# Optimization experiments

Measured on AMD Instinct MI355X. Metric: run time of the kernel, lower is better.

The kernel has to match this reference:

```python
import jax, jax.numpy as jnp
import numpy as np

NUM_CLASS = 1000
FEAT_DIM = 512
BATCH = 131072


def _safe_cdist(a, b):
    # Euclidean distance matrix, numerically safe sqrt (0 on the diagonal,
    # finite gradient), matching torch.cdist(p=2).
    a2 = jnp.sum(a * a, axis=-1, keepdims=True)        # [Na, 1]
    b2 = jnp.sum(b * b, axis=-1)                       # [Nb]
    d2 = jnp.maximum(a2 + b2 - 2.0 * (a @ b.T), 0.0)   # [Na, Nb]
    pos = d2 > 0
    return jnp.where(pos, jnp.sqrt(jnp.where(pos, d2, 1.0)), 0.0)


def setup_inputs() -> dict:
    key = jax.random.key(0)
    kf, kl, kc = jax.random.split(key, 3)
    features = jax.random.normal(kf, (BATCH, FEAT_DIM), dtype=jnp.float32)
    labels = jax.random.randint(kl, (BATCH,), 0, NUM_CLASS)
    center = jax.random.normal(kc, (NUM_CLASS, FEAT_DIM), dtype=jnp.float32)
    return {"features": features, "center": center, "labels": labels}


def reference(features, center, labels):
    # Threshold computed from the initial centers in __init__ (detached).
    init_dist = _safe_cdist(center, center)                     # [C, C]
    thres_inter = jax.lax.stop_gradient(jnp.mean(init_dist)) * 3.0

    # Per-class accumulation: the Python loops in the torch code are exactly
    # a segment-sum (scatter-add) of features into centers + a bincount.
    counts = jax.ops.segment_sum(
        jnp.ones((labels.shape[0],), dtype=features.dtype), labels,
        num_segments=NUM_CLASS)                                  # [C]
    sums = jax.ops.segment_sum(features, labels, num_segments=NUM_CLASS)  # [C, D]
    new_center = (center + sums) / jnp.maximum(counts, 1.0)[:, None]

    dist = _safe_cdist(new_center, new_center)                   # [C, C]
    hinge = jnp.where(dist < thres_inter, thres_inter - dist, 0.0)
    inter_loss = jnp.mean(hinge)
    # torch forward returns (inter_loss, self.center.data) -- center was
    # mutated in place, so it is the updated per-class mean center.
    return (inter_loss, new_center)
```

## Files before the change

kernel.cpp:

```cpp
#include <hip/hip_runtime.h>
#include <hip/hip_bf16.h>
#include <math.h>

#define BATCH   131072
#define NCLASS  1000
#define FDIM    512
#define NTILE   136
#define CAP     320

typedef __attribute__((ext_vector_type(4))) float f32x4;
typedef __attribute__((ext_vector_type(8))) short short8;

#define OFF_CURSOR   0
#define OFF_ACCS     4096
#define OFF_DONE     4104
#define OFF_PERM     8192
#define OFF_WSM      1290240
static_assert(OFF_PERM + NCLASS * CAP * 4 <= OFF_WSM, "perm/wsM overlap");
static_assert(OFF_ACCS >= OFF_CURSOR + 1024 * 4, "cursor/accs overlap");

__device__ __forceinline__ ushort f2bf(float x) {
    union { float f; unsigned u; } v; v.f = x;
    unsigned r = v.u + 0x7fff + ((v.u >> 16) & 1);
    return (ushort)(r >> 16);
}

template <int MODE>
__device__ void dist_mfma(const float* __restrict__ M, float th, int by, int bx,
                          float* __restrict__ accs) {
    __shared__ ushort Abf[64][72];
    __shared__ ushort Bbf[64][72];
    __shared__ float  rnA[64];
    __shared__ float  rnB[64];
    __shared__ float  red[256];

    const int tid  = threadIdx.x;
    const int lane = tid & 63;
    const int w    = tid >> 6;
    const int wr   = w >> 1, wc = w & 1;
    const int row4 = tid >> 2;
    const int cq   = tid & 3;
    const int gi_s = by * 64 + row4;
    const int gj_s = bx * 64 + row4;

    f32x4 acc[2][2];
#pragma unroll
    for (int m = 0; m < 2; ++m)
#pragma unroll
        for (int n = 0; n < 2; ++n) acc[m][n] = (f32x4){0.f, 0.f, 0.f, 0.f};

    float nA = 0.f, nB = 0.f;
    for (int k0 = 0; k0 < 8; ++k0) {
        __syncthreads();
#pragma unroll
        for (int c = 0; c < 4; ++c) {
            const int col  = cq * 16 + c * 4;
            const int gcol = k0 * 64 + col;
            f32x4 av = (f32x4){0.f, 0.f, 0.f, 0.f};
            f32x4 bv = (f32x4){0.f, 0.f, 0.f, 0.f};
            if (gi_s < NCLASS) av = *(const f32x4*)&M[(size_t)gi_s * FDIM + gcol];
            if (gj_s < NCLASS) bv = *(const f32x4*)&M[(size_t)gj_s * FDIM + gcol];
            nA += av.x * av.x + av.y * av.y + av.z * av.z + av.w * av.w;
            nB += bv.x * bv.x + bv.y * bv.y + bv.z * bv.z + bv.w * bv.w;
            ushort4 ap, bp;
            ap.x = f2bf(av.x); ap.y = f2bf(av.y); ap.z = f2bf(av.z); ap.w = f2bf(av.w);
            bp.x = f2bf(bv.x); bp.y = f2bf(bv.y); bp.z = f2bf(bv.z); bp.w = f2bf(bv.w);
            *(ushort4*)&Abf[row4][col] = ap;
            *(ushort4*)&Bbf[row4][col] = bp;
        }
        __syncthreads();
#pragma unroll
        for (int kk = 0; kk < 2; ++kk) {
            short8 a[2], b[2];
#pragma unroll
            for (int m = 0; m < 2; ++m)
                a[m] = *(const short8*)&Abf[wr * 32 + m * 16 + (lane & 15)]
                                          [kk * 32 + (lane >> 4) * 8];
#pragma unroll
            for (int n = 0; n < 2; ++n)
                b[n] = *(const short8*)&Bbf[wc * 32 + n * 16 + (lane & 15)]
                                          [kk * 32 + (lane >> 4) * 8];
#pragma unroll
            for (int m = 0; m < 2; ++m)
#pragma unroll
                for (int n = 0; n < 2; ++n)
                    acc[m][n] = __builtin_amdgcn_mfma_f32_16x16x32_bf16(
                        a[m], b[n], acc[m][n], 0, 0, 0);
        }
    }

    nA += __shfl_xor(nA, 1, 64); nA += __shfl_xor(nA, 2, 64);
    nB += __shfl_xor(nB, 1, 64); nB += __shfl_xor(nB, 2, 64);
    if (cq == 0) { rnA[row4] = nA; rnB[row4] = nB; }
    __syncthreads();

    float local = 0.f;
#pragma unroll
    for (int m = 0; m < 2; ++m)
#pragma unroll
        for (int n = 0; n < 2; ++n)
#pragma unroll
            for (int i = 0; i < 4; ++i) {
                const int r_l = wr * 32 + m * 16 + (lane >> 4) * 4 + i;
                const int c_l = wc * 32 + n * 16 + (lane & 15);
                const int gi = by * 64 + r_l;
                const int gj = bx * 64 + c_l;
                if (gi < NCLASS && gj < NCLASS && gj > gi) {
                    float d2 = rnA[r_l] + rnB[c_l] - 2.0f * acc[m][n][i];
                    d2 = fmaxf(d2, 0.0f);
                    float dst = (d2 > 0.0f) ? sqrtf(d2) : 0.0f;
                    if (MODE == 1) {
                        if (dst < th) local += th - dst;
                    } else {
                        local += dst;
                    }
                }
            }

    red[tid] = local;
    __syncthreads();
    for (int s = 128; s > 0; s >>= 1) {
        if (tid < s) red[tid] += red[tid + s];
        __syncthreads();
    }
    if (tid == 0) atomicAdd(&accs[MODE], red[0]);
}

__global__ __launch_bounds__(256)
void k2_scatter_dist0(const int* __restrict__ labels,
                      int* __restrict__ cursor0,
                      int* __restrict__ perm,
                      const float* __restrict__ center,
                      float* __restrict__ accs) {
    const int b = blockIdx.x, t = threadIdx.x;
    if (b >= BATCH / 1024) {
        int idx = b - BATCH / 1024;
        int by = 0;
        while (idx >= 16 - by) { idx -= 16 - by; ++by; }
        dist_mfma<0>(center, 0.0f, by, by + idx, accs);
        return;
    }
    const int gid = b * 256 + t;
    int4 l = ((const int4*)labels)[gid];
    const int r = gid * 4;
    perm[l.x * CAP + atomicAdd(&cursor0[l.x], 1)] = r + 0;
    perm[l.y * CAP + atomicAdd(&cursor0[l.y], 1)] = r + 1;
    perm[l.z * CAP + atomicAdd(&cursor0[l.z], 1)] = r + 2;
    perm[l.w * CAP + atomicAdd(&cursor0[l.w], 1)] = r + 3;
}

__global__ __launch_bounds__(512)
void k3_gather_finalize(const float* __restrict__ features,
                        const int* __restrict__ cursor0,
                        const int* __restrict__ perm,
                        const float* __restrict__ center,
                        float* __restrict__ out_center,
                        float* __restrict__ wsM) {
    const int c = blockIdx.x, t = threadIdx.x;
    const int par = t >> 7;
    const int pos = t & 127;
    const int n   = cursor0[c];
    const int* pp = perm + c * CAP;
    __shared__ float part[4][128][4];

    f32x4 acc = (f32x4){0.f, 0.f, 0.f, 0.f};
    int idx[8];
    int r = par;
    if (r + 28 < n) {
#pragma unroll
        for (int u = 0; u < 8; ++u) idx[u] = pp[r + 4 * u];
    }
    while (r + 28 < n) {
        const int nr = r + 32;
        int nidx[8];
        if (nr + 28 < n) {
#pragma unroll
            for (int u = 0; u < 8; ++u) nidx[u] = pp[nr + 4 * u];
        } else {
#pragma unroll
            for (int u = 0; u < 8; ++u) nidx[u] = 0;
        }
        f32x4 v0 = *(const f32x4*)&features[(size_t)idx[0] * FDIM + pos * 4];
        f32x4 v1 = *(const f32x4*)&features[(size_t)idx[1] * FDIM + pos * 4];
        f32x4 v2 = *(const f32x4*)&features[(size_t)idx[2] * FDIM + pos * 4];
        f32x4 v3 = *(const f32x4*)&features[(size_t)idx[3] * FDIM + pos * 4];
        f32x4 v4 = *(const f32x4*)&features[(size_t)idx[4] * FDIM + pos * 4];
        f32x4 v5 = *(const f32x4*)&features[(size_t)idx[5] * FDIM + pos * 4];
        f32x4 v6 = *(const f32x4*)&features[(size_t)idx[6] * FDIM + pos * 4];
        f32x4 v7 = *(const f32x4*)&features[(size_t)idx[7] * FDIM + pos * 4];
        acc += ((v0 + v1) + (v2 + v3)) + ((v4 + v5) + (v6 + v7));
#pragma unroll
        for (int u = 0; u < 8; ++u) idx[u] = nidx[u];
        r = nr;
    }
    for (; r < n; r += 4)
        acc += *(const f32x4*)&features[(size_t)pp[r] * FDIM + pos * 4];

    *(f32x4*)&part[par][pos][0] = acc;
    __syncthreads();
    if (t < 128) {
        f32x4 s = *(const f32x4*)&part[0][t][0];
        s += *(const f32x4*)&part[1][t][0];
        s += *(const f32x4*)&part[2][t][0];
        s += *(const f32x4*)&part[3][t][0];
        const f32x4 cc = *(const f32x4*)&center[(size_t)c * FDIM + t * 4];
        const float invn = 1.0f / fmaxf((float)n, 1.0f);
        const f32x4 nc = (cc + s) * invn;
        float* o = out_center + (size_t)c * FDIM + t * 4;
        o[0] = nc.x; o[1] = nc.y; o[2] = nc.z; o[3] = nc.w;
        *(f32x4*)&wsM[(size_t)c * FDIM + t * 4] = nc;
    }
}

__global__ __launch_bounds__(256)
void k5_dist1(const float* __restrict__ wsM, float* __restrict__ accs,
              int* __restrict__ done, float* __restrict__ out0) {
    int idx = blockIdx.x;
    int by = 0;
    while (idx >= 16 - by) { idx -= 16 - by; ++by; }
    const float th = 6.0f * accs[0] * 1e-6f;
    dist_mfma<1>(wsM, th, by, by + idx, accs);
    if (threadIdx.x == 0) {
        __threadfence();
        if (atomicAdd(done, 1) == NTILE - 1) {
            __threadfence();
            const float l1 = atomicAdd(&accs[1], 0.0f);
            const double thd = 6.0 * (double)accs[0] * 1e-6;
            out0[0] = (float)((2.0 * (double)l1 + (double)NCLASS * thd) * 1e-6);
        }
    }
}

extern "C" void kernel_launch(void* const* d_in, const int* in_sizes, int n_in,
                              void* d_out, int out_size, void* d_ws, size_t ws_size,
                              hipStream_t stream) {
    const float* features = (const float*)d_in[0];
    const float* center   = (const float*)d_in[1];
    const int*   labels   = (const int*)d_in[2];
    float* out = (float*)d_out;
    char*  ws  = (char*)d_ws;

    int*   cursor0 = (int*)(ws + OFF_CURSOR);
    float* accs    = (float*)(ws + OFF_ACCS);
    int*   done    = (int*)(ws + OFF_DONE);
    int*   perm    = (int*)(ws + OFF_PERM);
    float* wsM     = (float*)(ws + OFF_WSM);

    hipMemsetAsync(ws, 0, 4112, stream);
    k2_scatter_dist0<<<BATCH / 1024 + NTILE, 256, 0, stream>>>(labels, cursor0,
                                                               perm, center, accs);
    k3_gather_finalize<<<NCLASS, 512, 0, stream>>>(features, cursor0, perm,
                                                   center, out + 1, wsM);
    k5_dist1<<<NTILE, 256, 0, stream>>>(wsM, accs, done, out);
}
```

Measured before the change: 118.3 us.

## Split per-class gather into quarter work items via persistent atomic work queue

The per-class gather kernel now runs as 1024 persistent blocks that pull work items from a global atomic counter. Each item covers a quarter of one class's rows, which spreads uneven class sizes across blocks. Partial sums go into a zeroed global accumulator with float atomics, and a new small kernel applies the center add and the divide. The cost is a larger memset (about 2 MB), 2M float atomics, an extra launch, and a sum order that is no longer deterministic.

```diff
diff --git a/kernel.cpp b/kernel.cpp
--- a/kernel.cpp
+++ b/kernel.cpp
@@ -7,17 +7,22 @@
 #define FDIM    512
 #define NTILE   136
 #define CAP     320
+#define NITEMS  (4 * NCLASS)
+#define K3BLK   1024
 
 typedef __attribute__((ext_vector_type(4))) float f32x4;
 typedef __attribute__((ext_vector_type(8))) short short8;
 
-#define OFF_CURSOR   0
-#define OFF_ACCS     4096
-#define OFF_DONE     4104
-#define OFF_PERM     8192
-#define OFF_WSM      1290240
+#define OFF_QHEAD    0
+#define OFF_CURSOR   64
+#define OFF_ACCS     4160
+#define OFF_DONE     4168
+#define OFF_ACCBUF   8192
+#define OFF_PERM     2056192
+#define OFF_WSM      3336192
+static_assert(OFF_CURSOR + 1024 * 4 <= OFF_ACCS, "cursor/accs overlap");
+static_assert(OFF_ACCBUF + NCLASS * FDIM * 4 <= OFF_PERM, "accbuf/perm overlap");
 static_assert(OFF_PERM + NCLASS * CAP * 4 <= OFF_WSM, "perm/wsM overlap");
-static_assert(OFF_ACCS >= OFF_CURSOR + 1024 * 4, "cursor/accs overlap");
 
 __device__ __forceinline__ ushort f2bf(float x) {
     union { float f; unsigned u; } v; v.f = x;
@@ -150,66 +155,95 @@
 }
 
 __global__ __launch_bounds__(512)
-void k3_gather_finalize(const float* __restrict__ features,
+void k3_gather_balanced(const float* __restrict__ features,
                         const int* __restrict__ cursor0,
                         const int* __restrict__ perm,
-                        const float* __restrict__ center,
-                        float* __restrict__ out_center,
-                        float* __restrict__ wsM) {
-    const int c = blockIdx.x, t = threadIdx.x;
+                        int* __restrict__ qhead,
+                        float* __restrict__ accbuf) {
+    const int t   = threadIdx.x;
     const int par = t >> 7;
     const int pos = t & 127;
-    const int n   = cursor0[c];
-    const int* pp = perm + c * CAP;
+    __shared__ int   sItem;
     __shared__ float part[4][128][4];
 
-    f32x4 acc = (f32x4){0.f, 0.f, 0.f, 0.f};
-    int idx[8];
-    int r = par;
-    if (r + 28 < n) {
-#pragma unroll
-        for (int u = 0; u < 8; ++u) idx[u] = pp[r + 4 * u];
-    }
-    while (r + 28 < n) {
-        const int nr = r + 32;
-        int nidx[8];
-        if (nr + 28 < n) {
-#pragma unroll
-            for (int u = 0; u < 8; ++u) nidx[u] = pp[nr + 4 * u];
-        } else {
-#pragma unroll
-            for (int u = 0; u < 8; ++u) nidx[u] = 0;
-        }
-        f32x4 v0 = *(const f32x4*)&features[(size_t)idx[0] * FDIM + pos * 4];
-        f32x4 v1 = *(const f32x4*)&features[(size_t)idx[1] * FDIM + pos * 4];
-        f32x4 v2 = *(const f32x4*)&features[(size_t)idx[2] * FDIM + pos * 4];
-        f32x4 v3 = *(const f32x4*)&features[(size_t)idx[3] * FDIM + pos * 4];
-        f32x4 v4 = *(const f32x4*)&features[(size_t)idx[4] * FDIM + pos * 4];
-        f32x4 v5 = *(const f32x4*)&features[(size_t)idx[5] * FDIM + pos * 4];
-        f32x4 v6 = *(const f32x4*)&features[(size_t)idx[6] * FDIM + pos * 4];
-        f32x4 v7 = *(const f32x4*)&features[(size_t)idx[7] * FDIM + pos * 4];
-        acc += ((v0 + v1) + (v2 + v3)) + ((v4 + v5) + (v6 + v7));
-#pragma unroll
-        for (int u = 0; u < 8; ++u) idx[u] = nidx[u];
-        r = nr;
-    }
-    for (; r < n; r += 4)
-        acc += *(const f32x4*)&features[(size_t)pp[r] * FDIM + pos * 4];
-
-    *(f32x4*)&part[par][pos][0] = acc;
-    __syncthreads();
-    if (t < 128) {
-        f32x4 s = *(const f32x4*)&part[0][t][0];
-        s += *(const f32x4*)&part[1][t][0];
-        s += *(const f32x4*)&part[2][t][0];
-        s += *(const f32x4*)&part[3][t][0];
-        const f32x4 cc = *(const f32x4*)&center[(size_t)c * FDIM + t * 4];
-        const float invn = 1.0f / fmaxf((float)n, 1.0f);
-        const f32x4 nc = (cc + s) * invn;
-        float* o = out_center + (size_t)c * FDIM + t * 4;
-        o[0] = nc.x; o[1] = nc.y; o[2] = nc.z; o[3] = nc.w;
-        *(f32x4*)&wsM[(size_t)c * FDIM + t * 4] = nc;
-    }
+    for (;;) {
+        if (t == 0) sItem = atomicAdd(qhead, 1);
+        __syncthreads();
+        const int item = sItem;
+        if (item >= NITEMS) break;
+        const int c  = item % NCLASS;
+        const int qt = item / NCLASS;
+        const int n   = cursor0[c];
+        const int per = (n + 3) >> 2;
+        const int s0  = qt * per;
+        const int e0  = min(n, s0 + per);
+        const int cnt = e0 - s0;
+        const int* pp = perm + c * CAP + s0;
+
+        f32x4 acc = (f32x4){0.f, 0.f, 0.f, 0.f};
+        int idx[8];
+        int r = par;
+        if (r + 28 < cnt) {
+#pragma unroll
+            for (int u = 0; u < 8; ++u) idx[u] = pp[r + 4 * u];
+        }
+        while (r + 28 < cnt) {
+            const int nr = r + 32;
+            int nidx[8];
+            if (nr + 28 < cnt) {
+#pragma unroll
+                for (int u = 0; u < 8; ++u) nidx[u] = pp[nr + 4 * u];
+            } else {
+#pragma unroll
+                for (int u = 0; u < 8; ++u) nidx[u] = 0;
+            }
+            f32x4 v0 = *(const f32x4*)&features[(size_t)idx[0] * FDIM + pos * 4];
+            f32x4 v1 = *(const f32x4*)&features[(size_t)idx[1] * FDIM + pos * 4];
+            f32x4 v2 = *(const f32x4*)&features[(size_t)idx[2] * FDIM + pos * 4];
+            f32x4 v3 = *(const f32x4*)&features[(size_t)idx[3] * FDIM + pos * 4];
+            f32x4 v4 = *(const f32x4*)&features[(size_t)idx[4] * FDIM + pos * 4];
+            f32x4 v5 = *(const f32x4*)&features[(size_t)idx[5] * FDIM + pos * 4];
+            f32x4 v6 = *(const f32x4*)&features[(size_t)idx[6] * FDIM + pos * 4];
+            f32x4 v7 = *(const f32x4*)&features[(size_t)idx[7] * FDIM + pos * 4];
+            acc += ((v0 + v1) + (v2 + v3)) + ((v4 + v5) + (v6 + v7));
+#pragma unroll
+            for (int u = 0; u < 8; ++u) idx[u] = nidx[u];
+            r = nr;
+        }
+        for (; r < cnt; r += 4)
+            acc += *(const f32x4*)&features[(size_t)pp[r] * FDIM + pos * 4];
+
+        *(f32x4*)&part[par][pos][0] = acc;
+        __syncthreads();
+        if (t < 128) {
+            f32x4 s = *(const f32x4*)&part[0][t][0];
+            s += *(const f32x4*)&part[1][t][0];
+            s += *(const f32x4*)&part[2][t][0];
+            s += *(const f32x4*)&part[3][t][0];
+            float* dst = accbuf + (size_t)c * FDIM + t * 4;
+            atomicAdd(dst + 0, s.x);
+            atomicAdd(dst + 1, s.y);
+            atomicAdd(dst + 2, s.z);
+            atomicAdd(dst + 3, s.w);
+        }
+        __syncthreads();
+    }
+}
+
+__global__ __launch_bounds__(128)
+void k4_finalize(const float* __restrict__ center,
+                 const float* __restrict__ accbuf,
+                 const int* __restrict__ cursor0,
+                 float* __restrict__ out_center,
+                 float* __restrict__ wsM) {
+    const int c = blockIdx.x, t = threadIdx.x;
+    const f32x4 s  = *(const f32x4*)&accbuf[(size_t)c * FDIM + t * 4];
+    const f32x4 cc = *(const f32x4*)&center[(size_t)c * FDIM + t * 4];
+    const float invn = 1.0f / fmaxf((float)cursor0[c], 1.0f);
+    const f32x4 nc = (cc + s) * invn;
+    float* o = out_center + (size_t)c * FDIM + t * 4;
+    o[0] = nc.x; o[1] = nc.y; o[2] = nc.z; o[3] = nc.w;
+    *(f32x4*)&wsM[(size_t)c * FDIM + t * 4] = nc;
 }
 
 __global__ __launch_bounds__(256)
@@ -240,16 +274,19 @@
     float* out = (float*)d_out;
     char*  ws  = (char*)d_ws;
 
+    int*   qhead   = (int*)(ws + OFF_QHEAD);
     int*   cursor0 = (int*)(ws + OFF_CURSOR);
     float* accs    = (float*)(ws + OFF_ACCS);
     int*   done    = (int*)(ws + OFF_DONE);
+    float* accbuf  = (float*)(ws + OFF_ACCBUF);
     int*   perm    = (int*)(ws + OFF_PERM);
     float* wsM     = (float*)(ws + OFF_WSM);
 
-    hipMemsetAsync(ws, 0, 4112, stream);
+    hipMemsetAsync(ws, 0, OFF_ACCBUF + NCLASS * FDIM * 4, stream);
     k2_scatter_dist0<<<BATCH / 1024 + NTILE, 256, 0, stream>>>(labels, cursor0,
                                                                perm, center, accs);
-    k3_gather_finalize<<<NCLASS, 512, 0, stream>>>(features, cursor0, perm,
-                                                   center, out + 1, wsM);
+    k3_gather_balanced<<<K3BLK, 512, 0, stream>>>(features, cursor0, perm,
+                                                  qhead, accbuf);
+    k4_finalize<<<NCLASS, 128, 0, stream>>>(center, accbuf, cursor0, out + 1, wsM);
     k5_dist1<<<NTILE, 256, 0, stream>>>(wsM, accs, done, out);
 }
```

New measurement: 155.3 us. +31.3%, slower.

## Split per-class gather across two blocks and add separate finalize kernel

Applied to the files above, without the earlier changes.

The gather kernel now launches two blocks per class, each summing half of that class's feature rows into a partial buffer in workspace. A new small kernel then adds the two partials to the center, divides by the count, and writes the output and the workspace copy. The aim is more blocks in flight to hide memory latency during the gather, at the cost of an extra kernel launch and an extra round trip of about 4 MB of partial sums through global memory.

```diff
diff --git a/kernel.cpp b/kernel.cpp
--- a/kernel.cpp
+++ b/kernel.cpp
@@ -15,8 +15,10 @@
 #define OFF_ACCS     4096
 #define OFF_DONE     4104
 #define OFF_PERM     8192
-#define OFF_WSM      1290240
-static_assert(OFF_PERM + NCLASS * CAP * 4 <= OFF_WSM, "perm/wsM overlap");
+#define OFF_PBUF     1290240
+#define OFF_WSM      5386240
+static_assert(OFF_PERM + NCLASS * CAP * 4 <= OFF_PBUF, "perm/pbuf overlap");
+static_assert(OFF_PBUF + 2 * NCLASS * FDIM * 4 <= OFF_WSM, "pbuf/wsM overlap");
 static_assert(OFF_ACCS >= OFF_CURSOR + 1024 * 4, "cursor/accs overlap");
 
 __device__ __forceinline__ ushort f2bf(float x) {
@@ -150,30 +152,32 @@
 }
 
 __global__ __launch_bounds__(512)
-void k3_gather_finalize(const float* __restrict__ features,
-                        const int* __restrict__ cursor0,
-                        const int* __restrict__ perm,
-                        const float* __restrict__ center,
-                        float* __restrict__ out_center,
-                        float* __restrict__ wsM) {
-    const int c = blockIdx.x, t = threadIdx.x;
+void k3_gather(const float* __restrict__ features,
+               const int* __restrict__ cursor0,
+               const int* __restrict__ perm,
+               float* __restrict__ pbuf) {
+    const int c = blockIdx.x, h = blockIdx.y, t = threadIdx.x;
     const int par = t >> 7;
     const int pos = t & 127;
     const int n   = cursor0[c];
-    const int* pp = perm + c * CAP;
+    const int per = (n + 1) >> 1;
+    const int s0  = h * per;
+    const int e0  = min(n, s0 + per);
+    const int cnt = e0 - s0;
+    const int* pp = perm + c * CAP + s0;
     __shared__ float part[4][128][4];
 
     f32x4 acc = (f32x4){0.f, 0.f, 0.f, 0.f};
     int idx[8];
     int r = par;
-    if (r + 28 < n) {
+    if (r + 28 < cnt) {
 #pragma unroll
         for (int u = 0; u < 8; ++u) idx[u] = pp[r + 4 * u];
     }
-    while (r + 28 < n) {
+    while (r + 28 < cnt) {
         const int nr = r + 32;
         int nidx[8];
-        if (nr + 28 < n) {
+        if (nr + 28 < cnt) {
 #pragma unroll
             for (int u = 0; u < 8; ++u) nidx[u] = pp[nr + 4 * u];
         } else {
@@ -193,7 +197,7 @@
         for (int u = 0; u < 8; ++u) idx[u] = nidx[u];
         r = nr;
     }
-    for (; r < n; r += 4)
+    for (; r < cnt; r += 4)
         acc += *(const f32x4*)&features[(size_t)pp[r] * FDIM + pos * 4];
 
     *(f32x4*)&part[par][pos][0] = acc;
@@ -203,13 +207,25 @@
         s += *(const f32x4*)&part[1][t][0];
         s += *(const f32x4*)&part[2][t][0];
         s += *(const f32x4*)&part[3][t][0];
-        const f32x4 cc = *(const f32x4*)&center[(size_t)c * FDIM + t * 4];
-        const float invn = 1.0f / fmaxf((float)n, 1.0f);
-        const f32x4 nc = (cc + s) * invn;
-        float* o = out_center + (size_t)c * FDIM + t * 4;
-        o[0] = nc.x; o[1] = nc.y; o[2] = nc.z; o[3] = nc.w;
-        *(f32x4*)&wsM[(size_t)c * FDIM + t * 4] = nc;
-    }
+        *(f32x4*)&pbuf[((size_t)h * NCLASS + c) * FDIM + t * 4] = s;
+    }
+}
+
+__global__ __launch_bounds__(128)
+void k4_finalize(const float* __restrict__ center,
+                 const float* __restrict__ pbuf,
+                 const int* __restrict__ cursor0,
+                 float* __restrict__ out_center,
+                 float* __restrict__ wsM) {
+    const int c = blockIdx.x, t = threadIdx.x;
+    f32x4 s = *(const f32x4*)&pbuf[((size_t)0 * NCLASS + c) * FDIM + t * 4];
+    s += *(const f32x4*)&pbuf[((size_t)1 * NCLASS + c) * FDIM + t * 4];
+    const f32x4 cc = *(const f32x4*)&center[(size_t)c * FDIM + t * 4];
+    const float invn = 1.0f / fmaxf((float)cursor0[c], 1.0f);
+    const f32x4 nc = (cc + s) * invn;
+    float* o = out_center + (size_t)c * FDIM + t * 4;
+    o[0] = nc.x; o[1] = nc.y; o[2] = nc.z; o[3] = nc.w;
+    *(f32x4*)&wsM[(size_t)c * FDIM + t * 4] = nc;
 }
 
 __global__ __launch_bounds__(256)
@@ -244,12 +260,13 @@
     float* accs    = (float*)(ws + OFF_ACCS);
     int*   done    = (int*)(ws + OFF_DONE);
     int*   perm    = (int*)(ws + OFF_PERM);
+    float* pbuf    = (float*)(ws + OFF_PBUF);
     float* wsM     = (float*)(ws + OFF_WSM);
 
     hipMemsetAsync(ws, 0, 4112, stream);
     k2_scatter_dist0<<<BATCH / 1024 + NTILE, 256, 0, stream>>>(labels, cursor0,
                                                                perm, center, accs);
-    k3_gather_finalize<<<NCLASS, 512, 0, stream>>>(features, cursor0, perm,
-                                                   center, out + 1, wsM);
+    k3_gather<<<dim3(NCLASS, 2), 512, 0, stream>>>(features, cursor0, perm, pbuf);
+    k4_finalize<<<NCLASS, 128, 0, stream>>>(center, pbuf, cursor0, out + 1, wsM);
     k5_dist1<<<NTILE, 256, 0, stream>>>(wsM, accs, done, out);
 }
```

After: 119.2 us. No clear change (+0.7%).
